# Performance work log

Hardware: AMD Instinct MI355X
Metric: run time of the kernel (lower is better)

The kernel has to match this reference:

```python
import jax, jax.numpy as jnp
import numpy as np

N, E = 50000, 800000
NODE_IN, EDGE_IN = 32, 16
EMB, GEMB = 128, 128
H, C, L, B = 4, 32, 2, 8   # heads, per-head dim, layers, graphs
GAT_IN = NODE_IN + EMB      # skip_conn=True
NEG_SLOPE = 0.2
EPS = 1e-5


def layernorm(x, g, b):
    m = jnp.mean(x, -1, keepdims=True)
    v = jnp.mean((x - m) ** 2, -1, keepdims=True)
    return (x - m) / jnp.sqrt(v + EPS) * g + b


def setup_inputs() -> dict:
    key = jax.random.key(0)
    ks = jax.random.split(key, 24)
    s = 0.05
    return {
        "x": jax.random.normal(ks[0], (N, NODE_IN), jnp.float32),
        "edge_attr": jax.random.normal(ks[1], (E, EDGE_IN), jnp.float32),
        "W_in": jax.random.normal(ks[2], (NODE_IN, EMB), jnp.float32) * s,
        "b_in": jnp.zeros((EMB,), jnp.float32),
        "W_src": jax.random.normal(ks[3], (L, GAT_IN, H * C), jnp.float32) * s,
        "W_edge": jax.random.normal(ks[4], (L, EDGE_IN, H * C), jnp.float32) * s,
        "att_src": jax.random.normal(ks[5], (L, H, C), jnp.float32) * s,
        "att_dst": jax.random.normal(ks[6], (L, H, C), jnp.float32) * s,
        "att_edge": jax.random.normal(ks[7], (L, H, C), jnp.float32) * s,
        "gat_bias": jnp.zeros((L, H * C), jnp.float32),
        "ln_gamma": jnp.ones((L, EMB), jnp.float32),
        "ln_beta": jnp.zeros((L, EMB), jnp.float32),
        "W_out": jax.random.normal(ks[8], (EMB, EMB), jnp.float32) * s,
        "b_out": jnp.zeros((EMB,), jnp.float32),
        "ln_out_gamma": jnp.ones((EMB,), jnp.float32),
        "ln_out_beta": jnp.zeros((EMB,), jnp.float32),
        "W_g": jax.random.normal(ks[9], (EMB, GEMB), jnp.float32) * s,
        "b_g": jnp.zeros((GEMB,), jnp.float32),
        "g_gamma": jnp.ones((GEMB,), jnp.float32),
        "g_beta": jnp.zeros((GEMB,), jnp.float32),
        "edge_index": jax.random.randint(ks[10], (2, E), 0, N, jnp.int32),
        "batch": jnp.sort(jax.random.randint(ks[11], (N,), 0, B, jnp.int32)),
    }


def reference(x, edge_attr, W_in, b_in, W_src, W_edge, att_src, att_dst, att_edge,
              gat_bias, ln_gamma, ln_beta, W_out, b_out, ln_out_gamma, ln_out_beta,
              W_g, b_g, g_gamma, g_beta, edge_index, batch):
    # PyG GATConv adds self-loops with edge_attr fill_value='mean'
    loop = jnp.arange(N, dtype=edge_index.dtype)
    src = jnp.concatenate([edge_index[0], loop])   # [E2]
    dst = jnp.concatenate([edge_index[1], loop])   # [E2]
    ea = jnp.concatenate([edge_attr, jnp.broadcast_to(edge_attr.mean(0), (N, EDGE_IN))], 0)

    h = jax.nn.relu(x @ W_in + b_in)  # [N, EMB]
    for l in range(L):
        inp = jnp.concatenate([x, h], -1)                   # skip connection [N, GAT_IN]
        xs = (inp @ W_src[l]).reshape(N, H, C)              # projected nodes
        a_s = jnp.einsum('nhc,hc->nh', xs, att_src[l])
        a_d = jnp.einsum('nhc,hc->nh', xs, att_dst[l])
        ee = (ea @ W_edge[l]).reshape(-1, H, C)             # [E2, H, C]
        a_e = jnp.einsum('ehc,hc->eh', ee, att_edge[l])
        alpha = jax.nn.leaky_relu(a_s[src] + a_d[dst] + a_e, NEG_SLOPE)  # [E2, H]
        # segment softmax over incoming edges of each destination node
        amax = jax.ops.segment_max(alpha, dst, num_segments=N)
        ex = jnp.exp(alpha - amax[dst])
        denom = jax.ops.segment_sum(ex, dst, num_segments=N)
        w = ex / (denom[dst] + 1e-16)
        msg = xs[src] * w[:, :, None]                        # [E2, H, C]
        out = jax.ops.segment_sum(msg, dst, num_segments=N).reshape(N, H * C) + gat_bias[l]
        h = jax.nn.elu(layernorm(out, ln_gamma[l], ln_beta[l]))

    g = layernorm(jax.nn.relu(h @ W_g + b_g), g_gamma, g_beta)
    gsum = jax.ops.segment_sum(g, batch, num_segments=B)
    cnt = jax.ops.segment_sum(jnp.ones((N, 1), g.dtype), batch, num_segments=B)
    graph_embeddings = gsum / jnp.maximum(cnt, 1.0)

    node_embeddings = layernorm(jax.nn.relu(h @ W_out + b_out), ln_out_gamma, ln_out_beta)
    return node_embeddings, graph_embeddings
```

## Files before the change

### kernel.cpp

```cpp
#include <hip/hip_runtime.h>

#define N_NODES 50000
#define N_EDGES 800000
#define E2      850000
#define NODE_IN 32
#define EDGE_IN 16
#define EMB     128
#define GAT_IN  160
#define NLAYER  2
#define NGRAPH  8
#define NB32    1563
#define NB64    782
#define LOG2E   1.44269504088896340736f

#define NBUCK   98
#define CHUNK   4096
#define NCHUNK  208

#define GWT_SRC0 0
#define GWT_SRC1 20480
#define GWT_OUT  40960
#define GWT_G    57344
#define GWT_TOT  73728

typedef short bf16x8 __attribute__((ext_vector_type(8)));
typedef float f32x4 __attribute__((ext_vector_type(4)));

__device__ __forceinline__ unsigned int f2bf(float f) {
    unsigned int u = __float_as_uint(f);
    return (u + 0x7FFFu + ((u >> 16) & 1u)) >> 16;
}
__device__ __forceinline__ float bf2f(unsigned int h) {
    return __uint_as_float(h << 16);
}
__device__ __forceinline__ unsigned int pack2bf(float a, float b) {
    return f2bf(a) | (f2bf(b) << 16);
}

__global__ void zero_kernel(float* __restrict__ p, int n) {
    int i = blockIdx.x * blockDim.x + threadIdx.x;
    int stride = gridDim.x * blockDim.x;
    for (; i < n; i += stride) p[i] = 0.f;
}

__global__ __launch_bounds__(256) void mega_kernel(
    const int* __restrict__ edge_index, const float* __restrict__ edge_attr,
    const float* __restrict__ x, const float* __restrict__ W_in,
    const float* __restrict__ b_in,
    const float* __restrict__ Wsrc, const float* __restrict__ Wout,
    const float* __restrict__ Wg,
    int* __restrict__ hist, float* __restrict__ meta,
    unsigned int* __restrict__ h_bf, unsigned int* __restrict__ x_bf,
    unsigned short* __restrict__ gwt) {
    __shared__ float smem[32 * NODE_IN];
    int b = blockIdx.x, t = threadIdx.x;

    if (b < NCHUNK) {
        int* lh = (int*)smem;
        if (t < NBUCK) lh[t] = 0;
        __syncthreads();
        int c0 = b * CHUNK;
#pragma unroll
        for (int i = 0; i < CHUNK / 256; i++) {
            int e = c0 + i * 256 + t;
            if (e < E2) {
                int dst = (e < N_EDGES) ? edge_index[N_EDGES + e] : (e - N_EDGES);
                atomicAdd(&lh[dst >> 9], 1);
            }
        }
        __syncthreads();
        if (t < NBUCK) hist[t * NCHUNK + b] = lh[t];
    } else if (b < NCHUNK + 512) {
        if (t < 16) smem[t] = 0.f;
        __syncthreads();
        int gid = (b - NCHUNK) * 256 + t;
        int q = gid & 3;
        const float4* ea4 = (const float4*)edge_attr;
        float4 s = make_float4(0.f, 0.f, 0.f, 0.f);
        for (int j = gid; j < N_EDGES * 4; j += 512 * 256) {
            float4 v = ea4[j];
            s.x += v.x; s.y += v.y; s.z += v.z; s.w += v.w;
        }
        atomicAdd(&smem[q * 4 + 0], s.x);
        atomicAdd(&smem[q * 4 + 1], s.y);
        atomicAdd(&smem[q * 4 + 2], s.z);
        atomicAdd(&smem[q * 4 + 3], s.w);
        __syncthreads();
        if (t < 16) atomicAdd(&meta[t], smem[t]);
    } else if (b < NCHUNK + 512 + NB32) {
        float (*inp)[NODE_IN] = (float (*)[NODE_IN])smem;
        int n0 = (b - NCHUNK - 512) * 32;
        for (int i = t; i < 32 * NODE_IN; i += 256) {
            int r = i >> 5, c = i & 31;
            int n = min(n0 + r, N_NODES - 1);
            inp[r][c] = x[(size_t)n * NODE_IN + c];
        }
        __syncthreads();
        for (int i = t; i < 32 * 16; i += 256) {
            int r = i >> 4, c = i & 15;
            int n = n0 + r;
            if (n < N_NODES) x_bf[(size_t)n * 16 + c] = pack2bf(inp[r][2 * c], inp[r][2 * c + 1]);
        }
        int wave = t >> 6, lane = t & 63;
        int c0 = lane * 2, c1 = c0 + 1;
        const float2* W2 = (const float2*)W_in;
        float acc[8][2];
#pragma unroll
        for (int j = 0; j < 8; j++) { acc[j][0] = b_in[c0]; acc[j][1] = b_in[c1]; }
#pragma unroll 2
        for (int k4 = 0; k4 < NODE_IN / 4; k4++) {
            float4 v[8];
#pragma unroll
            for (int j = 0; j < 8; j++) v[j] = *(const float4*)&inp[wave * 8 + j][k4 * 4];
#pragma unroll
            for (int kk = 0; kk < 4; kk++) {
                float2 w = W2[(k4 * 4 + kk) * 64 + lane];
#pragma unroll
                for (int j = 0; j < 8; j++) {
                    float vv = (&v[j].x)[kk];
                    acc[j][0] += vv * w.x;
                    acc[j][1] += vv * w.y;
                }
            }
        }
#pragma unroll
        for (int j = 0; j < 8; j++) {
            int n = n0 + wave * 8 + j;
            if (n < N_NODES)
                h_bf[(size_t)n * 64 + lane] = pack2bf(fmaxf(acc[j][0], 0.f), fmaxf(acc[j][1], 0.f));
        }
    } else {
        int g = (b - NCHUNK - 512 - NB32) * 256 + t;
        const float* Wm;
        int base, gg;
        if (g < 5120) {
            int l = g / 2560;
            gg = g - l * 2560;
            Wm = Wsrc + (size_t)l * GAT_IN * EMB;
            base = l * 20480;
        } else if (g < 7168) {
            gg = g - 5120;
            Wm = Wout;
            base = GWT_OUT;
        } else {
            gg = g - 7168;
            Wm = Wg;
            base = GWT_G;
        }
        int lane = gg & 63, tmp = gg >> 6;
        int nt = tmp & 7, kc = tmp >> 3;
        int quad = lane >> 4, l16 = lane & 15;
        int col = nt * 16 + l16, k0 = kc * 32 + quad * 8;
        unsigned int u[4];
#pragma unroll
        for (int j = 0; j < 4; j++)
            u[j] = pack2bf(Wm[(size_t)(k0 + 2 * j) * EMB + col],
                           Wm[(size_t)(k0 + 2 * j + 1) * EMB + col]);
        *(uint4*)(gwt + base + (size_t)gg * 8) = make_uint4(u[0], u[1], u[2], u[3]);
    }
}

__global__ __launch_bounds__(256) void bucket_scan_kernel(int* __restrict__ hist,
                                                          int* __restrict__ btot) {
    __shared__ int sm[256];
    int k = blockIdx.x, t = threadIdx.x;
    int v = (t < NCHUNK) ? hist[k * NCHUNK + t] : 0;
    sm[t] = v;
    __syncthreads();
#pragma unroll
    for (int d = 1; d < 256; d <<= 1) {
        int u = (t >= d) ? sm[t - d] : 0;
        __syncthreads();
        sm[t] += u;
        __syncthreads();
    }
    if (t < NCHUNK) hist[k * NCHUNK + t] = sm[t] - v;
    if (t == 255) btot[k] = sm[255];
}

__global__ __launch_bounds__(256) void base_prep_kernel(const int* __restrict__ btot,
                                                        int* __restrict__ bucket_base,
                                                        const float* __restrict__ W_edge,
                                                        const float* __restrict__ att_edge,
                                                        float* __restrict__ meta) {
    __shared__ int sm[256];
    int t = threadIdx.x;
    int v = (t < NBUCK) ? btot[t] : 0;
    sm[t] = v;
    __syncthreads();
#pragma unroll
    for (int d = 1; d < 256; d <<= 1) {
        int u = (t >= d) ? sm[t - d] : 0;
        __syncthreads();
        sm[t] += u;
        __syncthreads();
    }
    if (t < NBUCK) bucket_base[t] = sm[t] - v;
    if (t == NBUCK - 1) bucket_base[NBUCK] = sm[t];

    if (t < EDGE_IN) meta[t] = meta[t] * (1.0f / (float)N_EDGES);
    __syncthreads();
    if (t < 128) {
        int l = t >> 6, k = (t >> 2) & 15, h = t & 3;
        const float* w = W_edge + ((size_t)l * EDGE_IN + k) * EMB + h * 32;
        const float* a = att_edge + (size_t)l * EMB + h * 32;
        float acc = 0.f;
#pragma unroll
        for (int c = 0; c < 32; c++) acc += w[c] * a[c];
        meta[16 + (l * 16 + k) * 4 + h] = acc * LOG2E;
    }
    __syncthreads();
    if (t < 8) {
        int l = t >> 2, h = t & 3;
        float acc = 0.f;
#pragma unroll
        for (int k = 0; k < EDGE_IN; k++) acc += meta[k] * meta[16 + (l * 16 + k) * 4 + h];
        meta[144 + t] = acc;
    }
}

__global__ __launch_bounds__(256) void scatter_bucket_kernel(const int* __restrict__ edge_index,
                                                             const int* __restrict__ hist,
                                                             const int* __restrict__ bucket_base,
                                                             int2* __restrict__ brec) {
    __shared__ int cur[NBUCK];
    int b = blockIdx.x, t = threadIdx.x;
    if (t < NBUCK) cur[t] = bucket_base[t] + hist[t * NCHUNK + b];
    __syncthreads();
    int c0 = b * CHUNK;
#pragma unroll
    for (int i = 0; i < CHUNK / 256; i++) {
        int e = c0 + i * 256 + t;
        if (e < E2) {
            int src, dst;
            if (e < N_EDGES) {
                src = edge_index[e];
                dst = edge_index[N_EDGES + e];
            } else {
                src = dst = e - N_EDGES;
            }
            int pos = atomicAdd(&cur[dst >> 9], 1);
            brec[pos] = make_int2(src | ((dst & 511) << 16), e);
        }
    }
}

__global__ __launch_bounds__(512) void local_sort_kernel(const int* __restrict__ bucket_base,
                                                         const int2* __restrict__ brec,
                                                         const float* __restrict__ edge_attr,
                                                         const float* __restrict__ meta,
                                                         int* __restrict__ off,
                                                         int* __restrict__ csr_src,
                                                         float* __restrict__ csr_ae0,
                                                         float* __restrict__ csr_ae1) {
    __shared__ int lh[512];
    __shared__ int sm[512];
    __shared__ float Ml[128];
    __shared__ float loop_ae[8];
    int k = blockIdx.x, t = threadIdx.x;
    if (t < 128) Ml[t] = meta[16 + t];
    if (t < 8) loop_ae[t] = meta[144 + t];
    int base = bucket_base[k], end = bucket_base[k + 1], cnt = end - base;
    lh[t] = 0;
    __syncthreads();
    for (int i = t; i < cnt; i += 512) {
        int2 r = brec[base + i];
        atomicAdd(&lh[(r.x >> 16) & 511], 1);
    }
    __syncthreads();
    int v = lh[t];
    sm[t] = v;
    __syncthreads();
#pragma unroll
    for (int d = 1; d < 512; d <<= 1) {
        int u = (t >= d) ? sm[t - d] : 0;
        __syncthreads();
        sm[t] += u;
        __syncthreads();
    }
    int excl = sm[t] - v;
    int dst = (k << 9) + t;
    if (dst < N_NODES) off[dst] = base + excl;
    if (k == NBUCK - 1 && t == 0) off[N_NODES] = E2;
    lh[t] = excl;
    __syncthreads();
    for (int i = t; i < cnt; i += 512) {
        int2 r = brec[base + i];
        int dl = (r.x >> 16) & 511;
        int p = atomicAdd(&lh[dl], 1);
        int pos = base + p;
        int src = r.x & 0xFFFF;
        int e = r.y;
        csr_src[pos] = src;
        float ae[2][4];
        if (e < N_EDGES) {
            const float4* r4 = (const float4*)(edge_attr + (size_t)e * EDGE_IN);
#pragma unroll
            for (int l = 0; l < 2; l++)
#pragma unroll
                for (int hh = 0; hh < 4; hh++) ae[l][hh] = 0.f;
#pragma unroll
            for (int q = 0; q < 4; q++) {
                float4 vv = r4[q];
#pragma unroll
                for (int l = 0; l < 2; l++) {
                    const float* M = Ml + l * 64;
#pragma unroll
                    for (int hh = 0; hh < 4; hh++) {
                        ae[l][hh] += vv.x * M[(4 * q + 0) * 4 + hh] + vv.y * M[(4 * q + 1) * 4 + hh] +
                                     vv.z * M[(4 * q + 2) * 4 + hh] + vv.w * M[(4 * q + 3) * 4 + hh];
                    }
                }
            }
        } else {
#pragma unroll
            for (int l = 0; l < 2; l++)
#pragma unroll
                for (int hh = 0; hh < 4; hh++) ae[l][hh] = loop_ae[l * 4 + hh];
        }
        *(float4*)(csr_ae0 + (size_t)pos * 4) = make_float4(ae[0][0], ae[0][1], ae[0][2], ae[0][3]);
        *(float4*)(csr_ae1 + (size_t)pos * 4) = make_float4(ae[1][0], ae[1][1], ae[1][2], ae[1][3]);
    }
}

template <int K, int MODE>
__global__ __launch_bounds__(256) void dense_mfma_kernel(
    const unsigned int* __restrict__ xbf, const unsigned int* __restrict__ hbf,
    const unsigned short* __restrict__ gwt, const float* __restrict__ bias,
    const float* __restrict__ v1, const float* __restrict__ v2,
    const int* __restrict__ batch,
    unsigned int* __restrict__ xs_out, float* __restrict__ a_s, float* __restrict__ a_d,
    float* __restrict__ out_nodes, float* __restrict__ gsum, float* __restrict__ gcnt,
    const float* __restrict__ bias2, const float* __restrict__ v1b,
    const float* __restrict__ v2b) {
    constexpr int CLS = 132;
    __shared__ __align__(16) float cl[64 * CLS];
    __shared__ float red[(MODE != 0) ? 64 : 1][8];
    __shared__ float locw[(MODE == 3) ? 4 : 1][2][EMB];
    __shared__ int bids[(MODE == 3) ? 64 : 1];

    int t = threadIdx.x;
    int mode = MODE;
    int blk = blockIdx.x;
    if (MODE == 3) {
        mode = (blockIdx.x < NB64) ? 1 : 2;
        blk = (mode == 1) ? blockIdx.x : blockIdx.x - NB64;
    }
    int n0 = blk * 64;
    const unsigned short* gw = gwt;
    const float* bias_ = bias;
    const float* v1_ = v1;
    const float* v2_ = v2;
    if (MODE == 3 && mode == 2) {
        gw = gwt + (GWT_G - GWT_OUT);
        bias_ = bias2; v1_ = v1b; v2_ = v2b;
    }
    if (MODE == 3 && mode == 2 && t < 64) bids[t] = batch[min(n0 + t, N_NODES - 1)];

    int wave = t >> 6, lane = t & 63;
    int quad = lane >> 4, l16 = lane & 15;
    int arow = min(n0 + wave * 16 + l16, N_NODES - 1);
    const bf16x8* B = (const bf16x8*)gw;
    f32x4 acc[8];
#pragma unroll
    for (int i = 0; i < 8; i++) acc[i] = (f32x4){0.f, 0.f, 0.f, 0.f};
#pragma unroll
    for (int kc = 0; kc < K / 32; kc++) {
        bf16x8 af;
        if (MODE == 0 && kc == 0) {
            af = *(const bf16x8*)(xbf + (size_t)arow * 16 + quad * 4);
        } else {
            int hk = ((MODE == 0) ? (kc - 1) : kc) * 16;
            af = *(const bf16x8*)(hbf + (size_t)arow * 64 + hk + quad * 4);
        }
#pragma unroll
        for (int nt = 0; nt < 8; nt++) {
            bf16x8 bfv = B[(kc * 8 + nt) * 64 + lane];
            acc[nt] = __builtin_amdgcn_mfma_f32_16x16x32_bf16(af, bfv, acc[nt], 0, 0, 0);
        }
    }
#pragma unroll
    for (int nt = 0; nt < 8; nt++) {
#pragma unroll
        for (int i = 0; i < 4; i++) {
            int r = wave * 16 + quad * 4 + i;
            cl[r * CLS + nt * 16 + l16] = acc[nt][i];
        }
    }
    __syncthreads();

    int p = t & 3, r = t >> 2;
    int n = n0 + r;
    const float4* c4 = (const float4*)(cl + r * CLS + p * 32);

    if (MODE == 0) {
        const float4* s4 = (const float4*)(v1_ + p * 32);
        const float4* d4 = (const float4*)(v2_ + p * 32);
        if (n < N_NODES) {
            float s_ = 0.f, d_ = 0.f;
#pragma unroll
            for (int i = 0; i < 8; i++) {
                float4 cv = c4[i], sv = s4[i], dv = d4[i];
                s_ += cv.x * sv.x + cv.y * sv.y + cv.z * sv.z + cv.w * sv.w;
                d_ += cv.x * dv.x + cv.y * dv.y + cv.z * dv.z + cv.w * dv.w;
                uint2 pk = make_uint2(pack2bf(cv.x, cv.y), pack2bf(cv.z, cv.w));
                *(uint2*)(xs_out + (size_t)n * 64 + p * 16 + 2 * i) = pk;
            }
            a_s[(size_t)n * 4 + p] = s_ * LOG2E;
            a_d[(size_t)n * 4 + p] = d_ * LOG2E;
        }
    } else {
        const float4* b4 = (const float4*)(bias_ + p * 32);
        float vals[32];
        float s_ = 0.f, q_ = 0.f;
#pragma unroll
        for (int i = 0; i < 8; i++) {
            float4 cv = c4[i], bv = b4[i];
            float w0 = fmaxf(cv.x + bv.x, 0.f), w1 = fmaxf(cv.y + bv.y, 0.f);
            float w2 = fmaxf(cv.z + bv.z, 0.f), w3 = fmaxf(cv.w + bv.w, 0.f);
            vals[4 * i] = w0; vals[4 * i + 1] = w1; vals[4 * i + 2] = w2; vals[4 * i + 3] = w3;
            s_ += w0 + w1 + w2 + w3;
            q_ += w0 * w0 + w1 * w1 + w2 * w2 + w3 * w3;
        }
        red[r][p] = s_;
        red[r][4 + p] = q_;
        __syncthreads();
        float sm = red[r][0] + red[r][1] + red[r][2] + red[r][3];
        float sq = red[r][4] + red[r][5] + red[r][6] + red[r][7];
        float mean = sm * (1.f / EMB);
        float var = sq * (1.f / EMB) - mean * mean;
        float rstd = rsqrtf(var + 1e-5f);
        const float4* g4 = (const float4*)(v1_ + p * 32);
        const float4* be4 = (const float4*)(v2_ + p * 32);
#pragma unroll
        for (int i = 0; i < 8; i++) {
            float4 gv = g4[i], bv = be4[i];
            vals[4 * i]     = (vals[4 * i]     - mean) * rstd * gv.x + bv.x;
            vals[4 * i + 1] = (vals[4 * i + 1] - mean) * rstd * gv.y + bv.y;
            vals[4 * i + 2] = (vals[4 * i + 2] - mean) * rstd * gv.z + bv.z;
            vals[4 * i + 3] = (vals[4 * i + 3] - mean) * rstd * gv.w + bv.w;
        }
        if (mode == 1) {
            if (n < N_NODES) {
                float* op = out_nodes + (size_t)n * EMB + p * 32;
#pragma unroll
                for (int i = 0; i < 8; i++)
                    *(float4*)(op + 4 * i) = make_float4(vals[4 * i], vals[4 * i + 1],
                                                         vals[4 * i + 2], vals[4 * i + 3]);
            }
        } else {
            int nvalid = min(64, N_NODES - n0);
            int bmin = bids[0], bmax = bids[nvalid - 1];
            int bid = bids[r];
            bool inA = (bid == bmin) && (n < N_NODES);
            bool inB = (bid == bmax) && (bmax != bmin) && (n < N_NODES);
            if (n < N_NODES && bid != bmin && bid != bmax) {
#pragma unroll
                for (int i = 0; i < 32; i++)
                    atomicAdd(&gsum[(size_t)bid * EMB + p * 32 + i], vals[i]);
            }
#pragma unroll
            for (int g = 0; g < 2; g++) {
                bool m = g ? inB : inA;
#pragma unroll
                for (int i = 0; i < 32; i++) {
                    float v = m ? vals[i] : 0.f;
                    v += __shfl_xor(v, 4, 64);
                    v += __shfl_xor(v, 8, 64);
                    v += __shfl_xor(v, 16, 64);
                    v += __shfl_xor(v, 32, 64);
                    if ((lane >> 2) == 0) locw[wave][g][(lane & 3) * 32 + i] = v;
                }
            }
            __syncthreads();
            if (t < 128) {
                float sA = locw[0][0][t] + locw[1][0][t] + locw[2][0][t] + locw[3][0][t];
                atomicAdd(&gsum[(size_t)bmin * EMB + t], sA);
                if (bmax != bmin) {
                    float sB = locw[0][1][t] + locw[1][1][t] + locw[2][1][t] + locw[3][1][t];
                    atomicAdd(&gsum[(size_t)bmax * EMB + t], sB);
                }
            } else if (t == 255) {
                int cA = 0, cB = 0;
                for (int rr = 0; rr < nvalid; rr++) {
                    int bb = bids[rr];
                    if (bb == bmin) cA++;
                    else if (bb == bmax) cB++;
                    else atomicAdd(&gcnt[bb], 1.f);
                }
                atomicAdd(&gcnt[bmin], (float)cA);
                if (bmax != bmin && cB > 0) atomicAdd(&gcnt[bmax], (float)cB);
            }
        }
    }
}

__global__ __launch_bounds__(256) void gat_gather_kernel(const int* __restrict__ off,
                                                         const int* __restrict__ csr_src,
                                                         const float* __restrict__ csr_ae,
                                                         const unsigned int* __restrict__ xs,
                                                         const float* __restrict__ a_s,
                                                         const float* __restrict__ a_d,
                                                         const float* __restrict__ bias_l,
                                                         const float* __restrict__ gamma_l,
                                                         const float* __restrict__ beta_l,
                                                         unsigned int* __restrict__ h_bf) {
    int t = threadIdx.x, wave = t >> 6, lane = t & 63;
    int n = blockIdx.x * 4 + wave;
    int g = lane >> 4, l16 = lane & 15;
    int h = l16 >> 2;
    float ad = a_d[n * 4 + h];
    int p0 = __builtin_amdgcn_readfirstlane(off[n]);
    int p1 = __builtin_amdgcn_readfirstlane(off[n + 1]);
    float den = 0.f;
    float acc[8];
#pragma unroll
    for (int j = 0; j < 8; j++) acc[j] = 0.f;

#define ACCUM8(X, EX)                                          \
    acc[0] += EX * __uint_as_float(X.x << 16);                 \
    acc[1] += EX * __uint_as_float(X.x & 0xFFFF0000u);         \
    acc[2] += EX * __uint_as_float(X.y << 16);                 \
    acc[3] += EX * __uint_as_float(X.y & 0xFFFF0000u);         \
    acc[4] += EX * __uint_as_float(X.z << 16);                 \
    acc[5] += EX * __uint_as_float(X.z & 0xFFFF0000u);         \
    acc[6] += EX * __uint_as_float(X.w << 16);                 \
    acc[7] += EX * __uint_as_float(X.w & 0xFFFF0000u);

    int niter = (p1 - p0) >> 3;
    int pb = p0;
    int sA = 0, sB = 0;
    float aeA = 0.f, aeB = 0.f;
    if (niter > 0) {
        int pA = pb + g, pB = pA + 4;
        sA = csr_src[pA];
        sB = csr_src[pB];
        aeA = csr_ae[pA * 4 + h];
        aeB = csr_ae[pB * 4 + h];
    }
    for (int it = 0; it < niter; it++) {
        int sA0 = sA, sB0 = sB;
        float aeA0 = aeA, aeB0 = aeB;
        pb += 8;
        if (it + 1 < niter) {
            int pA = pb + g, pB = pA + 4;
            sA = csr_src[pA];
            sB = csr_src[pB];
            aeA = csr_ae[pA * 4 + h];
            aeB = csr_ae[pB * 4 + h];
        }
        float asA = a_s[sA0 * 4 + h];
        float asB = a_s[sB0 * 4 + h];
        uint4 xA = *(const uint4*)(xs + (sA0 * 64 + l16 * 4));
        uint4 xB = *(const uint4*)(xs + (sB0 * 64 + l16 * 4));
        float alA = asA + ad + aeA0;
        alA = fmaxf(alA, 0.2f * alA);
        float exA = exp2f(alA);
        float alB = asB + ad + aeB0;
        alB = fmaxf(alB, 0.2f * alB);
        float exB = exp2f(alB);
        den += exA + exB;
        ACCUM8(xA, exA)
        ACCUM8(xB, exB)
    }
    if (pb < p1) {
        int plast = p1 - 1;
        int qA = pb + g, qB = pb + 4 + g;
        int pA = min(qA, plast), pB = min(qB, plast);
        int tsA = csr_src[pA], tsB = csr_src[pB];
        float aeA1 = csr_ae[pA * 4 + h];
        float aeB1 = csr_ae[pB * 4 + h];
        float asA = a_s[tsA * 4 + h];
        float asB = a_s[tsB * 4 + h];
        uint4 xA = *(const uint4*)(xs + (tsA * 64 + l16 * 4));
        uint4 xB = *(const uint4*)(xs + (tsB * 64 + l16 * 4));
        float alA = asA + ad + aeA1;
        alA = fmaxf(alA, 0.2f * alA);
        float exA = (qA <= plast) ? exp2f(alA) : 0.f;
        float alB = asB + ad + aeB1;
        alB = fmaxf(alB, 0.2f * alB);
        float exB = (qB <= plast) ? exp2f(alB) : 0.f;
        den += exA + exB;
        ACCUM8(xA, exA)
        ACCUM8(xB, exB)
    }
#undef ACCUM8

#pragma unroll
    for (int j = 0; j < 8; j++) {
        acc[j] += __shfl_xor(acc[j], 16, 64);
        acc[j] += __shfl_xor(acc[j], 32, 64);
    }
    den += __shfl_xor(den, 16, 64);
    den += __shfl_xor(den, 32, 64);

    float dinv = 1.0f / (den + 1e-16f);
    int c0 = l16 * 8;
    const float4* b4 = (const float4*)(bias_l + c0);
    float4 bv0 = b4[0], bv1 = b4[1];
    float v[8];
    v[0] = acc[0] * dinv + bv0.x; v[1] = acc[1] * dinv + bv0.y;
    v[2] = acc[2] * dinv + bv0.z; v[3] = acc[3] * dinv + bv0.w;
    v[4] = acc[4] * dinv + bv1.x; v[5] = acc[5] * dinv + bv1.y;
    v[6] = acc[6] * dinv + bv1.z; v[7] = acc[7] * dinv + bv1.w;
    float sm = 0.f, sq = 0.f;
#pragma unroll
    for (int j = 0; j < 8; j++) { sm += v[j]; sq += v[j] * v[j]; }
#pragma unroll
    for (int o = 1; o <= 8; o <<= 1) {
        sm += __shfl_xor(sm, o, 64);
        sq += __shfl_xor(sq, o, 64);
    }
    float mean = sm * (1.f / EMB);
    float var = sq * (1.f / EMB) - mean * mean;
    float rstd = rsqrtf(var + 1e-5f);
    const float4* g4 = (const float4*)(gamma_l + c0);
    const float4* be4 = (const float4*)(beta_l + c0);
    float4 gv0 = g4[0], gv1 = g4[1], bev0 = be4[0], bev1 = be4[1];
    float y[8];
    y[0] = (v[0] - mean) * rstd * gv0.x + bev0.x;
    y[1] = (v[1] - mean) * rstd * gv0.y + bev0.y;
    y[2] = (v[2] - mean) * rstd * gv0.z + bev0.z;
    y[3] = (v[3] - mean) * rstd * gv0.w + bev0.w;
    y[4] = (v[4] - mean) * rstd * gv1.x + bev1.x;
    y[5] = (v[5] - mean) * rstd * gv1.y + bev1.y;
    y[6] = (v[6] - mean) * rstd * gv1.z + bev1.z;
    y[7] = (v[7] - mean) * rstd * gv1.w + bev1.w;
#pragma unroll
    for (int j = 0; j < 8; j++) y[j] = y[j] > 0.f ? y[j] : __expf(y[j]) - 1.f;
    if (g == 0) {
        uint4 o4;
        o4.x = pack2bf(y[0], y[1]);
        o4.y = pack2bf(y[2], y[3]);
        o4.z = pack2bf(y[4], y[5]);
        o4.w = pack2bf(y[6], y[7]);
        *(uint4*)(h_bf + (size_t)n * 64 + l16 * 4) = o4;
    }
}

__global__ void graph_out_kernel(const float* __restrict__ gsum, const float* __restrict__ gcnt,
                                 float* __restrict__ out) {
    int i = blockIdx.x * blockDim.x + threadIdx.x;
    if (i >= NGRAPH * EMB) return;
    int b = i >> 7;
    float c = fmaxf(gcnt[b], 1.f);
    out[(size_t)N_NODES * EMB + i] = gsum[i] / c;
}

extern "C" void kernel_launch(void* const* d_in, const int* in_sizes, int n_in,
                              void* d_out, int out_size, void* d_ws, size_t ws_size,
                              hipStream_t stream) {
    (void)in_sizes; (void)n_in; (void)out_size; (void)ws_size;
    const float* x         = (const float*)d_in[0];
    const float* edge_attr = (const float*)d_in[1];
    const float* W_in      = (const float*)d_in[2];
    const float* b_in      = (const float*)d_in[3];
    const float* W_src     = (const float*)d_in[4];
    const float* W_edge    = (const float*)d_in[5];
    const float* att_src   = (const float*)d_in[6];
    const float* att_dst   = (const float*)d_in[7];
    const float* att_edge  = (const float*)d_in[8];
    const float* gat_bias  = (const float*)d_in[9];
    const float* ln_gamma  = (const float*)d_in[10];
    const float* ln_beta   = (const float*)d_in[11];
    const float* W_out     = (const float*)d_in[12];
    const float* b_out     = (const float*)d_in[13];
    const float* ln_og     = (const float*)d_in[14];
    const float* ln_ob     = (const float*)d_in[15];
    const float* W_g       = (const float*)d_in[16];
    const float* b_g       = (const float*)d_in[17];
    const float* g_gamma   = (const float*)d_in[18];
    const float* g_beta    = (const float*)d_in[19];
    const int* edge_index  = (const int*)d_in[20];
    const int* batch       = (const int*)d_in[21];
    float* out = (float*)d_out;

    float* ws              = (float*)d_ws;
    unsigned int* h_bf     = (unsigned int*)ws;
    unsigned int* xs       = h_bf + (size_t)N_NODES * 64;
    unsigned int* x_bf     = xs + (size_t)N_NODES * 64;
    float* a_s             = (float*)(x_bf + (size_t)N_NODES * 16);
    float* a_d             = a_s + (size_t)N_NODES * 4;
    float* csr_ae          = a_d + (size_t)N_NODES * 4;
    unsigned short* gwt    = (unsigned short*)(csr_ae + (size_t)2 * E2 * 4);
    float* meta            = (float*)(gwt + GWT_TOT);
    float* gsum            = meta + 152;
    float* gcnt            = gsum + NGRAPH * EMB;
    int*   off             = (int*)(gcnt + NGRAPH);
    int*   csr_src         = off + N_NODES + 2;
    int2*  brec            = (int2*)(csr_src + E2);
    int*   hist            = (int*)(brec + E2);
    int*   btot            = hist + NBUCK * NCHUNK;
    int*   bucket_base     = btot + NBUCK;

    zero_kernel<<<8, 256, 0, stream>>>(meta, 152 + NGRAPH * EMB + NGRAPH);
    mega_kernel<<<NCHUNK + 512 + NB32 + 36, 256, 0, stream>>>(
        edge_index, edge_attr, x, W_in, b_in, W_src, W_out, W_g,
        hist, meta, h_bf, x_bf, gwt);

    bucket_scan_kernel<<<NBUCK, 256, 0, stream>>>(hist, btot);
    base_prep_kernel<<<1, 256, 0, stream>>>(btot, bucket_base, W_edge, att_edge, meta);
    scatter_bucket_kernel<<<NCHUNK, 256, 0, stream>>>(edge_index, hist, bucket_base, brec);
    local_sort_kernel<<<NBUCK, 512, 0, stream>>>(bucket_base, brec, edge_attr, meta,
                                                 off, csr_src, csr_ae,
                                                 csr_ae + (size_t)E2 * 4);

    for (int l = 0; l < NLAYER; l++) {
        dense_mfma_kernel<GAT_IN, 0><<<NB64, 256, 0, stream>>>(
            x_bf, h_bf, gwt + (l ? GWT_SRC1 : GWT_SRC0), nullptr,
            att_src + (size_t)l * EMB, att_dst + (size_t)l * EMB, nullptr,
            xs, a_s, a_d, nullptr, nullptr, nullptr, nullptr, nullptr, nullptr);
        gat_gather_kernel<<<N_NODES / 4, 256, 0, stream>>>(
            off, csr_src, csr_ae + (size_t)l * E2 * 4, xs, a_s, a_d,
            gat_bias + (size_t)l * EMB, ln_gamma + (size_t)l * EMB,
            ln_beta + (size_t)l * EMB, h_bf);
    }

    dense_mfma_kernel<EMB, 3><<<2 * NB64, 256, 0, stream>>>(
        nullptr, h_bf, gwt + GWT_OUT, b_out, ln_og, ln_ob, batch,
        nullptr, nullptr, nullptr, out, gsum, gcnt, b_g, g_gamma, g_beta);
    graph_out_kernel<<<4, 256, 0, stream>>>(gsum, gcnt, out);
}
```

Before: 418.1 us.

## Split edge-attention projection out of local sort; replace graph-sum atomics with partials

The local sort kernel, which runs only 98 blocks, now writes just a permutation of (src, edge id) pairs. A new wide kernel reads that permutation and computes csr_src plus the per-layer edge attention terms, spreading the edge_attr gather and matvec across thousands of blocks. Separately, the graph pooling step no longer does atomicAdds into gsum. Each block writes per-block partial sums with graph ids, and graph_out_kernel reduces them serially over 782 entries. This adds a kernel launch and an extra round trip through the permutation buffer, which reuses the xs workspace.

```diff
diff --git a/kernel.cpp b/kernel.cpp
--- a/kernel.cpp
+++ b/kernel.cpp
@@ -11,6 +11,7 @@
 #define NGRAPH  8
 #define NB32    1563
 #define NB64    782
+#define EB      3321
 #define LOG2E   1.44269504088896340736f
 
 #define NBUCK   98
@@ -247,19 +248,11 @@
 
 __global__ __launch_bounds__(512) void local_sort_kernel(const int* __restrict__ bucket_base,
                                                          const int2* __restrict__ brec,
-                                                         const float* __restrict__ edge_attr,
-                                                         const float* __restrict__ meta,
                                                          int* __restrict__ off,
-                                                         int* __restrict__ csr_src,
-                                                         float* __restrict__ csr_ae0,
-                                                         float* __restrict__ csr_ae1) {
+                                                         int2* __restrict__ perm) {
     __shared__ int lh[512];
     __shared__ int sm[512];
-    __shared__ float Ml[128];
-    __shared__ float loop_ae[8];
     int k = blockIdx.x, t = threadIdx.x;
-    if (t < 128) Ml[t] = meta[16 + t];
-    if (t < 8) loop_ae[t] = meta[144 + t];
     int base = bucket_base[k], end = bucket_base[k + 1], cnt = end - base;
     lh[t] = 0;
     __syncthreads();
@@ -288,39 +281,55 @@
         int2 r = brec[base + i];
         int dl = (r.x >> 16) & 511;
         int p = atomicAdd(&lh[dl], 1);
-        int pos = base + p;
-        int src = r.x & 0xFFFF;
-        int e = r.y;
-        csr_src[pos] = src;
-        float ae[2][4];
-        if (e < N_EDGES) {
-            const float4* r4 = (const float4*)(edge_attr + (size_t)e * EDGE_IN);
-#pragma unroll
-            for (int l = 0; l < 2; l++)
-#pragma unroll
-                for (int hh = 0; hh < 4; hh++) ae[l][hh] = 0.f;
-#pragma unroll
-            for (int q = 0; q < 4; q++) {
-                float4 vv = r4[q];
-#pragma unroll
-                for (int l = 0; l < 2; l++) {
-                    const float* M = Ml + l * 64;
-#pragma unroll
-                    for (int hh = 0; hh < 4; hh++) {
-                        ae[l][hh] += vv.x * M[(4 * q + 0) * 4 + hh] + vv.y * M[(4 * q + 1) * 4 + hh] +
-                                     vv.z * M[(4 * q + 2) * 4 + hh] + vv.w * M[(4 * q + 3) * 4 + hh];
-                    }
+        perm[base + p] = make_int2(r.x & 0xFFFF, r.y);
+    }
+}
+
+__global__ __launch_bounds__(256) void compute_ae_kernel(const int2* __restrict__ perm,
+                                                         const float* __restrict__ edge_attr,
+                                                         const float* __restrict__ meta,
+                                                         int* __restrict__ csr_src,
+                                                         float* __restrict__ csr_ae0,
+                                                         float* __restrict__ csr_ae1) {
+    __shared__ float Ml[128];
+    __shared__ float loop_ae[8];
+    int t = threadIdx.x;
+    if (t < 128) Ml[t] = meta[16 + t];
+    if (t < 8) loop_ae[t] = meta[144 + t];
+    __syncthreads();
+    int p = blockIdx.x * 256 + t;
+    if (p >= E2) return;
+    int2 pe = perm[p];
+    int src = pe.x, e = pe.y;
+    csr_src[p] = src;
+    float ae[2][4];
+    if (e < N_EDGES) {
+        const float4* r4 = (const float4*)(edge_attr + (size_t)e * EDGE_IN);
+#pragma unroll
+        for (int l = 0; l < 2; l++)
+#pragma unroll
+            for (int hh = 0; hh < 4; hh++) ae[l][hh] = 0.f;
+#pragma unroll
+        for (int q = 0; q < 4; q++) {
+            float4 v = r4[q];
+#pragma unroll
+            for (int l = 0; l < 2; l++) {
+                const float* M = Ml + l * 64;
+#pragma unroll
+                for (int hh = 0; hh < 4; hh++) {
+                    ae[l][hh] += v.x * M[(4 * q + 0) * 4 + hh] + v.y * M[(4 * q + 1) * 4 + hh] +
+                                 v.z * M[(4 * q + 2) * 4 + hh] + v.w * M[(4 * q + 3) * 4 + hh];
                 }
             }
-        } else {
-#pragma unroll
-            for (int l = 0; l < 2; l++)
-#pragma unroll
-                for (int hh = 0; hh < 4; hh++) ae[l][hh] = loop_ae[l * 4 + hh];
-        }
-        *(float4*)(csr_ae0 + (size_t)pos * 4) = make_float4(ae[0][0], ae[0][1], ae[0][2], ae[0][3]);
-        *(float4*)(csr_ae1 + (size_t)pos * 4) = make_float4(ae[1][0], ae[1][1], ae[1][2], ae[1][3]);
-    }
+        }
+    } else {
+#pragma unroll
+        for (int l = 0; l < 2; l++)
+#pragma unroll
+            for (int hh = 0; hh < 4; hh++) ae[l][hh] = loop_ae[l * 4 + hh];
+    }
+    *(float4*)(csr_ae0 + (size_t)p * 4) = make_float4(ae[0][0], ae[0][1], ae[0][2], ae[0][3]);
+    *(float4*)(csr_ae1 + (size_t)p * 4) = make_float4(ae[1][0], ae[1][1], ae[1][2], ae[1][3]);
 }
 
 template <int K, int MODE>
@@ -332,7 +341,8 @@
     unsigned int* __restrict__ xs_out, float* __restrict__ a_s, float* __restrict__ a_d,
     float* __restrict__ out_nodes, float* __restrict__ gsum, float* __restrict__ gcnt,
     const float* __restrict__ bias2, const float* __restrict__ v1b,
-    const float* __restrict__ v2b) {
+    const float* __restrict__ v2b,
+    float* __restrict__ gpartA, float* __restrict__ gpartB, int* __restrict__ gids) {
     constexpr int CLS = 132;
     __shared__ __align__(16) float cl[64 * CLS];
     __shared__ float red[(MODE != 0) ? 64 : 1][8];
@@ -475,11 +485,14 @@
             __syncthreads();
             if (t < 128) {
                 float sA = locw[0][0][t] + locw[1][0][t] + locw[2][0][t] + locw[3][0][t];
-                atomicAdd(&gsum[(size_t)bmin * EMB + t], sA);
+                gpartA[(size_t)blk * EMB + t] = sA;
                 if (bmax != bmin) {
                     float sB = locw[0][1][t] + locw[1][1][t] + locw[2][1][t] + locw[3][1][t];
-                    atomicAdd(&gsum[(size_t)bmax * EMB + t], sB);
+                    gpartB[(size_t)blk * EMB + t] = sB;
                 }
+            } else if (t == 128) {
+                gids[2 * blk] = bmin;
+                gids[2 * blk + 1] = (bmax != bmin) ? bmax : -1;
             } else if (t == 255) {
                 int cA = 0, cB = 0;
                 for (int rr = 0; rr < nvalid; rr++) {
@@ -638,13 +651,22 @@
     }
 }
 
-__global__ void graph_out_kernel(const float* __restrict__ gsum, const float* __restrict__ gcnt,
-                                 float* __restrict__ out) {
-    int i = blockIdx.x * blockDim.x + threadIdx.x;
-    if (i >= NGRAPH * EMB) return;
-    int b = i >> 7;
-    float c = fmaxf(gcnt[b], 1.f);
-    out[(size_t)N_NODES * EMB + i] = gsum[i] / c;
+__global__ __launch_bounds__(128) void graph_out_kernel(const float* __restrict__ gsum,
+                                                        const float* __restrict__ gcnt,
+                                                        const float* __restrict__ gpartA,
+                                                        const float* __restrict__ gpartB,
+                                                        const int* __restrict__ gids,
+                                                        float* __restrict__ out) {
+    int b = blockIdx.x;
+    int c = threadIdx.x;
+    float s = gsum[(size_t)b * EMB + c];
+    for (int k = 0; k < NB64; k++) {
+        int2 id = ((const int2*)gids)[k];
+        if (id.x == b) s += gpartA[(size_t)k * EMB + c];
+        if (id.y == b) s += gpartB[(size_t)k * EMB + c];
+    }
+    float cnt = fmaxf(gcnt[b], 1.f);
+    out[(size_t)N_NODES * EMB + (size_t)b * EMB + c] = s / cnt;
 }
 
 extern "C" void kernel_launch(void* const* d_in, const int* in_sizes, int n_in,
@@ -692,6 +714,10 @@
     int*   hist            = (int*)(brec + E2);
     int*   btot            = hist + NBUCK * NCHUNK;
     int*   bucket_base     = btot + NBUCK;
+    float* gpartA          = (float*)(bucket_base + NBUCK + 2);
+    float* gpartB          = gpartA + (size_t)NB64 * EMB;
+    int*   gids            = (int*)(gpartB + (size_t)NB64 * EMB);
+    int2*  perm            = (int2*)xs;
 
     zero_kernel<<<8, 256, 0, stream>>>(meta, 152 + NGRAPH * EMB + NGRAPH);
     mega_kernel<<<NCHUNK + 512 + NB32 + 36, 256, 0, stream>>>(
@@ -701,15 +727,16 @@
     bucket_scan_kernel<<<NBUCK, 256, 0, stream>>>(hist, btot);
     base_prep_kernel<<<1, 256, 0, stream>>>(btot, bucket_base, W_edge, att_edge, meta);
     scatter_bucket_kernel<<<NCHUNK, 256, 0, stream>>>(edge_index, hist, bucket_base, brec);
-    local_sort_kernel<<<NBUCK, 512, 0, stream>>>(bucket_base, brec, edge_attr, meta,
-                                                 off, csr_src, csr_ae,
-                                                 csr_ae + (size_t)E2 * 4);
+    local_sort_kernel<<<NBUCK, 512, 0, stream>>>(bucket_base, brec, off, perm);
+    compute_ae_kernel<<<EB, 256, 0, stream>>>(perm, edge_attr, meta,
+                                              csr_src, csr_ae, csr_ae + (size_t)E2 * 4);
 
     for (int l = 0; l < NLAYER; l++) {
         dense_mfma_kernel<GAT_IN, 0><<<NB64, 256, 0, stream>>>(
             x_bf, h_bf, gwt + (l ? GWT_SRC1 : GWT_SRC0), nullptr,
             att_src + (size_t)l * EMB, att_dst + (size_t)l * EMB, nullptr,
-            xs, a_s, a_d, nullptr, nullptr, nullptr, nullptr, nullptr, nullptr);
+            xs, a_s, a_d, nullptr, nullptr, nullptr, nullptr, nullptr, nullptr,
+            nullptr, nullptr, nullptr);
         gat_gather_kernel<<<N_NODES / 4, 256, 0, stream>>>(
             off, csr_src, csr_ae + (size_t)l * E2 * 4, xs, a_s, a_d,
             gat_bias + (size_t)l * EMB, ln_gamma + (size_t)l * EMB,
@@ -718,6 +745,7 @@
 
     dense_mfma_kernel<EMB, 3><<<2 * NB64, 256, 0, stream>>>(
         nullptr, h_bf, gwt + GWT_OUT, b_out, ln_og, ln_ob, batch,
-        nullptr, nullptr, nullptr, out, gsum, gcnt, b_g, g_gamma, g_beta);
-    graph_out_kernel<<<4, 256, 0, stream>>>(gsum, gcnt, out);
-}
+        nullptr, nullptr, nullptr, out, gsum, gcnt, b_g, g_gamma, g_beta,
+        gpartA, gpartB, gids);
+    graph_out_kernel<<<NGRAPH, 128, 0, stream>>>(gsum, gcnt, gpartA, gpartB, gids, out);
+}
```

Result: slower. 469.8 us (+12.4%).
